# Performance work log

Hardware: AMD Instinct MI355X
Metric: run time of the kernel (lower is better)

Reference implementation:

```python
import jax, jax.numpy as jnp
import numpy as np


def setup_inputs() -> dict:
    key = jax.random.key(0)
    kx, kq, kk, kv = jax.random.split(key, 4)
    d_model, d_head = 1024, 64
    x = jax.random.normal(kx, (4, 4096, d_model), dtype=jnp.float32)
    scale = 1.0 / np.sqrt(d_model)
    Wq = jax.random.normal(kq, (d_model, d_head), dtype=jnp.float32) * scale
    Wk = jax.random.normal(kk, (d_model, d_head), dtype=jnp.float32) * scale
    Wv = jax.random.normal(kv, (d_model, d_head), dtype=jnp.float32) * scale
    return {"x": x, "Wq": Wq, "Wk": Wk, "Wv": Wv}


def reference(x, Wq, Wk, Wv):
    # x: [B, S, D]; Wq/Wk/Wv: [D, H]
    d_head = Wq.shape[-1]
    Q = jnp.einsum('bsd,dh->bsh', x, Wq)
    K = jnp.einsum('bsd,dh->bsh', x, Wk)
    V = jnp.einsum('bsd,dh->bsh', x, Wv)
    scores = jnp.einsum('bqh,bkh->bqk', Q, K) / jnp.sqrt(jnp.float32(d_head))
    S = x.shape[1]
    causal = jnp.tril(jnp.ones((S, S), dtype=bool))  # [S, S]
    scores = jnp.where(causal, scores, -jnp.inf)
    weights = jax.nn.softmax(scores, axis=-1)  # [B, S, S]
    return jnp.einsum('bqk,bkh->bqh', weights, V)
```

## Files before the change

### kernel.cpp

```cpp
#include <hip/hip_runtime.h>

#define D_MODEL 1024
#define D_HEAD  64
#define SEQ     4096
#define BATCH   4
#define M_TOT   (BATCH * SEQ)
#define LOG2E   1.44269504088896f
#define MFIX_L2 17.3123404906676f

typedef __bf16 bf16;
typedef bf16  bf16x8 __attribute__((ext_vector_type(8)));
typedef float f32x4  __attribute__((ext_vector_type(4)));

#define MFMA(a, b, c) __builtin_amdgcn_mfma_f32_16x16x32_bf16(a, b, c, 0, 0, 0)

#define QKV_OFF 0
#define OBUF_OFF 6291456
#define LBUF_OFF 10485760
#define WT_OFF   10551296

__global__ void zero_kernel(float4* __restrict__ p, int n4)
{
    int i = blockIdx.x * 256 + threadIdx.x;
    if (i < n4) p[i] = float4{0.f, 0.f, 0.f, 0.f};
}

__global__ void wt_kernel(const float* __restrict__ Wq, const float* __restrict__ Wk,
                          const float* __restrict__ Wv, bf16* __restrict__ Wt)
{
    const int bx = blockIdx.x;
    const int wm = bx >> 6, n = bx & 63;
    const float* W = (wm == 0) ? Wq : (wm == 1) ? Wk : Wv;
    #pragma unroll
    for (int j = 0; j < 4; j++) {
        int k = threadIdx.x + j * 256;
        Wt[(size_t)bx * D_MODEL + k] = (bf16)W[(size_t)k * D_HEAD + n];
    }
}

#define XP 40

__global__ __launch_bounds__(256) void proj_kernel(
    const float* __restrict__ x, const bf16* __restrict__ Wt,
    bf16* __restrict__ qkv)
{
    __shared__ __align__(16) bf16 xs[64][XP];
    __shared__ __align__(16) bf16 ws[192][XP];

    const int t    = threadIdx.x;
    const int wv   = t >> 6;
    const int lane = t & 63;
    const int quad = lane >> 4;
    const int l15  = lane & 15;
    const int bm   = blockIdx.x;

    const int xrow = t >> 2;
    const int xk8  = (t & 3) * 8;
    const float* xg = x + (size_t)(bm * 64 + xrow) * D_MODEL + xk8;

    f32x4 acc[12] = {};

    float4 xa = *(const float4*)(xg);
    float4 xb = *(const float4*)(xg + 4);

    for (int k0 = 0; k0 < D_MODEL; k0 += 32) {
        bf16x8 xv;
        xv[0] = (bf16)xa.x; xv[1] = (bf16)xa.y; xv[2] = (bf16)xa.z; xv[3] = (bf16)xa.w;
        xv[4] = (bf16)xb.x; xv[5] = (bf16)xb.y; xv[6] = (bf16)xb.z; xv[7] = (bf16)xb.w;
        *(bf16x8*)&xs[xrow][xk8] = xv;
        #pragma unroll
        for (int it = 0; it < 3; it++) {
            int id = t + it * 256;
            int n = id >> 2, kk8 = (id & 3) * 8;
            *(bf16x8*)&ws[n][kk8] =
                *(const bf16x8*)(Wt + (size_t)n * D_MODEL + k0 + kk8);
        }
        __syncthreads();

        if (k0 + 32 < D_MODEL) {
            xa = *(const float4*)(xg + k0 + 32);
            xb = *(const float4*)(xg + k0 + 36);
        }

        bf16x8 a = *(bf16x8*)&xs[wv * 16 + l15][quad * 8];
        #pragma unroll
        for (int t4 = 0; t4 < 12; t4++) {
            bf16x8 b = *(bf16x8*)&ws[t4 * 16 + l15][quad * 8];
            acc[t4] = MFMA(a, b, acc[t4]);
        }
        __syncthreads();
    }

    #pragma unroll
    for (int t4 = 0; t4 < 12; t4++) {
        const int wm = t4 >> 2;
        const float sc = (wm == 0) ? 0.125f : 1.0f;
        const int h = (t4 & 3) * 16 + l15;
        bf16* outp = qkv + (size_t)wm * M_TOT * D_HEAD;
        #pragma unroll
        for (int r = 0; r < 4; r++) {
            int m = bm * 64 + wv * 16 + quad * 4 + r;
            outp[(size_t)m * D_HEAD + h] = (bf16)(acc[t4][r] * sc);
        }
    }
}

#define TS 72

__global__ __launch_bounds__(256) void attn_kernel(
    const bf16* __restrict__ qkv, float* __restrict__ o_buf,
    float* __restrict__ l_buf)
{
    __shared__ __align__(16) bf16 Ks[64][TS];
    __shared__ __align__(16) bf16 Vs[64][TS];
    __shared__ __align__(16) bf16 Ps[4][16][TS];

    const int i = blockIdx.x;
    const int c = blockIdx.y;
    const int b = blockIdx.z;
    const int ntiles = i + 1;
    const int tile0  = c * 8;
    if (tile0 >= ntiles) return;
    const int tile1 = min(tile0 + 8, ntiles);

    const bf16* Q = qkv;
    const bf16* K = qkv + (size_t)M_TOT * D_HEAD;
    const bf16* V = qkv + (size_t)2 * M_TOT * D_HEAD;

    const int t    = threadIdx.x;
    const int wv   = t >> 6;
    const int lane = t & 63;
    const int quad = lane >> 4;
    const int l15  = lane & 15;
    const int qb   = i * 64;
    const size_t base = (size_t)b * SEQ * D_HEAD;

    bf16x8 qf0, qf1;
    {
        const bf16* qr = Q + base + (size_t)(qb + wv * 16 + l15) * D_HEAD;
        qf0 = *(const bf16x8*)(qr + quad * 8);
        qf1 = *(const bf16x8*)(qr + 32 + quad * 8);
    }

    f32x4 o[4] = {};
    float l_r[4] = {};
    const int qw0 = qb + wv * 16;

    const int krow = t >> 2;
    const int kq8  = (t & 3) * 8;
    const int vdim = t & 63;

    for (int tile = tile0; tile < tile1; tile++) {
        const int kk0 = tile * 64;
        {
            const bf16* kp = K + base + (size_t)(kk0 + krow) * D_HEAD;
            *(bf16x8*)&Ks[krow][kq8]      = *(const bf16x8*)(kp + kq8);
            *(bf16x8*)&Ks[krow][kq8 + 32] = *(const bf16x8*)(kp + kq8 + 32);
        }
        #pragma unroll
        for (int h = 0; h < 2; h++) {
            const int kk = (t >> 6) * 8 + h * 32;
            bf16x8 vvv;
            #pragma unroll
            for (int j = 0; j < 8; j++)
                vvv[j] = V[base + (size_t)(kk0 + kk + j) * D_HEAD + vdim];
            *(bf16x8*)&Vs[vdim][kk] = vvv;
        }
        __syncthreads();

        f32x4 sc4[4];
        #pragma unroll
        for (int kt = 0; kt < 4; kt++) {
            f32x4 z = {};
            z = MFMA(qf0, *(bf16x8*)&Ks[kt * 16 + l15][quad * 8],      z);
            z = MFMA(qf1, *(bf16x8*)&Ks[kt * 16 + l15][32 + quad * 8], z);
            sc4[kt] = z;
        }

        const bool need_mask = (tile == i);

        #pragma unroll
        for (int r = 0; r < 4; r++) {
            #pragma unroll
            for (int kt = 0; kt < 4; kt++) {
                float s = sc4[kt][r];
                if (need_mask && (kk0 + kt * 16 + l15 > qw0 + quad * 4 + r))
                    s = -1e30f;
                float p = __builtin_amdgcn_exp2f(fmaf(s, LOG2E, -MFIX_L2));
                l_r[r] += p;
                Ps[wv][quad * 4 + r][kt * 16 + l15] = (bf16)p;
            }
        }
        __syncthreads();

        #pragma unroll
        for (int c2 = 0; c2 < 2; c2++) {
            bf16x8 pa = *(bf16x8*)&Ps[wv][l15][c2 * 32 + quad * 8];
            #pragma unroll
            for (int t4 = 0; t4 < 4; t4++) {
                bf16x8 vb = *(bf16x8*)&Vs[t4 * 16 + l15][c2 * 32 + quad * 8];
                o[t4] = MFMA(pa, vb, o[t4]);
            }
        }
        __syncthreads();
    }

    const int mrow0 = b * SEQ + qw0;
    #pragma unroll
    for (int r = 0; r < 4; r++) {
        float ls = l_r[r];
        #pragma unroll
        for (int sh = 1; sh < 16; sh <<= 1)
            ls += __shfl_xor(ls, sh, 64);
        if (l15 == 0)
            atomicAdd(&l_buf[mrow0 + quad * 4 + r], ls);
        const size_t orow = (size_t)(mrow0 + quad * 4 + r) * D_HEAD;
        #pragma unroll
        for (int t4 = 0; t4 < 4; t4++)
            atomicAdd(&o_buf[orow + t4 * 16 + l15], o[t4][r]);
    }
}

__global__ void norm_kernel(const float4* __restrict__ o_buf,
                            const float* __restrict__ l_buf,
                            float4* __restrict__ out)
{
    int gid = blockIdx.x * 256 + threadIdx.x;
    int m = gid >> 4;
    float inv = 1.0f / l_buf[m];
    float4 v = o_buf[gid];
    out[gid] = float4{v.x * inv, v.y * inv, v.z * inv, v.w * inv};
}

extern "C" void kernel_launch(void* const* d_in, const int* in_sizes, int n_in,
                              void* d_out, int out_size, void* d_ws, size_t ws_size,
                              hipStream_t stream) {
    const float* x  = (const float*)d_in[0];
    const float* Wq = (const float*)d_in[1];
    const float* Wk = (const float*)d_in[2];
    const float* Wv = (const float*)d_in[3];

    bf16*  qkv   = (bf16*)((char*)d_ws + QKV_OFF);
    float* o_buf = (float*)((char*)d_ws + OBUF_OFF);
    float* l_buf = (float*)((char*)d_ws + LBUF_OFF);
    bf16*  Wt    = (bf16*)((char*)d_ws + WT_OFF);

    const int zero4 = (M_TOT * 65) / 4;
    zero_kernel<<<(zero4 + 255) / 256, 256, 0, stream>>>((float4*)o_buf, zero4);
    wt_kernel<<<192, 256, 0, stream>>>(Wq, Wk, Wv, Wt);
    proj_kernel<<<M_TOT / 64, 256, 0, stream>>>(x, Wt, qkv);
    attn_kernel<<<dim3(SEQ / 64, 8, BATCH), 256, 0, stream>>>(qkv, o_buf, l_buf);
    norm_kernel<<<M_TOT * 16 / 256, 256, 0, stream>>>((const float4*)o_buf, l_buf,
                                                      (float4*)d_out);
}
```

Baseline: 173.0 us.

## Drop LDS from projection and shrink attention KV chunk for more blocks

The projection kernel becomes a single-wavefront block over 16 rows. Weight fragments are loaded straight from global memory into registers with a one-step prefetch, which removes the shared-memory staging and barriers. The attention split-KV chunk drops from 8 to 4 tiles, and the grid's y dimension grows to 16 so more blocks run in parallel. The cost is that each projection block rereads the full weight matrix from cache, and the smaller chunks mean more atomic adds into the output and row-sum buffers.

```diff
diff --git a/kernel.cpp b/kernel.cpp
--- a/kernel.cpp
+++ b/kernel.cpp
@@ -7,6 +7,7 @@
 #define M_TOT   (BATCH * SEQ)
 #define LOG2E   1.44269504088896f
 #define MFIX_L2 17.3123404906676f
+#define CHUNK   4
 
 typedef __bf16 bf16;
 typedef bf16  bf16x8 __attribute__((ext_vector_type(8)));
@@ -38,57 +39,48 @@
     }
 }
 
-#define XP 40
-
-__global__ __launch_bounds__(256) void proj_kernel(
+__global__ __launch_bounds__(64) void proj_kernel(
     const float* __restrict__ x, const bf16* __restrict__ Wt,
     bf16* __restrict__ qkv)
 {
-    __shared__ __align__(16) bf16 xs[64][XP];
-    __shared__ __align__(16) bf16 ws[192][XP];
-
-    const int t    = threadIdx.x;
-    const int wv   = t >> 6;
-    const int lane = t & 63;
+    const int lane = threadIdx.x;
     const int quad = lane >> 4;
     const int l15  = lane & 15;
-    const int bm   = blockIdx.x;
-
-    const int xrow = t >> 2;
-    const int xk8  = (t & 3) * 8;
-    const float* xg = x + (size_t)(bm * 64 + xrow) * D_MODEL + xk8;
+    const int row0 = blockIdx.x * 16;
+
+    const float* xr = x + (size_t)(row0 + l15) * D_MODEL + quad * 8;
+    const bf16*  wp = Wt + (size_t)l15 * D_MODEL + quad * 8;
 
     f32x4 acc[12] = {};
 
-    float4 xa = *(const float4*)(xg);
-    float4 xb = *(const float4*)(xg + 4);
+    float4 xa = *(const float4*)(xr);
+    float4 xb = *(const float4*)(xr + 4);
+    bf16x8 bf[12];
+    #pragma unroll
+    for (int t4 = 0; t4 < 12; t4++)
+        bf[t4] = *(const bf16x8*)(wp + (size_t)(t4 * 16) * D_MODEL);
 
     for (int k0 = 0; k0 < D_MODEL; k0 += 32) {
-        bf16x8 xv;
-        xv[0] = (bf16)xa.x; xv[1] = (bf16)xa.y; xv[2] = (bf16)xa.z; xv[3] = (bf16)xa.w;
-        xv[4] = (bf16)xb.x; xv[5] = (bf16)xb.y; xv[6] = (bf16)xb.z; xv[7] = (bf16)xb.w;
-        *(bf16x8*)&xs[xrow][xk8] = xv;
-        #pragma unroll
-        for (int it = 0; it < 3; it++) {
-            int id = t + it * 256;
-            int n = id >> 2, kk8 = (id & 3) * 8;
-            *(bf16x8*)&ws[n][kk8] =
-                *(const bf16x8*)(Wt + (size_t)n * D_MODEL + k0 + kk8);
-        }
-        __syncthreads();
-
-        if (k0 + 32 < D_MODEL) {
-            xa = *(const float4*)(xg + k0 + 32);
-            xb = *(const float4*)(xg + k0 + 36);
-        }
-
-        bf16x8 a = *(bf16x8*)&xs[wv * 16 + l15][quad * 8];
-        #pragma unroll
-        for (int t4 = 0; t4 < 12; t4++) {
-            bf16x8 b = *(bf16x8*)&ws[t4 * 16 + l15][quad * 8];
-            acc[t4] = MFMA(a, b, acc[t4]);
-        }
-        __syncthreads();
+        bf16x8 a;
+        a[0] = (bf16)xa.x; a[1] = (bf16)xa.y; a[2] = (bf16)xa.z; a[3] = (bf16)xa.w;
+        a[4] = (bf16)xb.x; a[5] = (bf16)xb.y; a[6] = (bf16)xb.z; a[7] = (bf16)xb.w;
+
+        bf16x8 bn[12];
+        const int k1 = k0 + 32;
+        if (k1 < D_MODEL) {
+            xa = *(const float4*)(xr + k1);
+            xb = *(const float4*)(xr + k1 + 4);
+            #pragma unroll
+            for (int t4 = 0; t4 < 12; t4++)
+                bn[t4] = *(const bf16x8*)(wp + (size_t)(t4 * 16) * D_MODEL + k1);
+        }
+
+        #pragma unroll
+        for (int t4 = 0; t4 < 12; t4++)
+            acc[t4] = MFMA(a, bf[t4], acc[t4]);
+
+        #pragma unroll
+        for (int t4 = 0; t4 < 12; t4++) bf[t4] = bn[t4];
     }
 
     #pragma unroll
@@ -99,7 +91,7 @@
         bf16* outp = qkv + (size_t)wm * M_TOT * D_HEAD;
         #pragma unroll
         for (int r = 0; r < 4; r++) {
-            int m = bm * 64 + wv * 16 + quad * 4 + r;
+            int m = row0 + quad * 4 + r;
             outp[(size_t)m * D_HEAD + h] = (bf16)(acc[t4][r] * sc);
         }
     }
@@ -111,17 +103,17 @@
     const bf16* __restrict__ qkv, float* __restrict__ o_buf,
     float* __restrict__ l_buf)
 {
-    __shared__ __align__(16) bf16 Ks[64][TS];
-    __shared__ __align__(16) bf16 Vs[64][TS];
-    __shared__ __align__(16) bf16 Ps[4][16][TS];
-
     const int i = blockIdx.x;
     const int c = blockIdx.y;
     const int b = blockIdx.z;
     const int ntiles = i + 1;
-    const int tile0  = c * 8;
+    const int tile0  = c * CHUNK;
     if (tile0 >= ntiles) return;
-    const int tile1 = min(tile0 + 8, ntiles);
+    const int tile1 = min(tile0 + CHUNK, ntiles);
+
+    __shared__ __align__(16) bf16 Ks[64][TS];
+    __shared__ __align__(16) bf16 Vs[64][TS];
+    __shared__ __align__(16) bf16 Ps[4][16][TS];
 
     const bf16* Q = qkv;
     const bf16* K = qkv + (size_t)M_TOT * D_HEAD;
@@ -248,8 +240,9 @@
     const int zero4 = (M_TOT * 65) / 4;
     zero_kernel<<<(zero4 + 255) / 256, 256, 0, stream>>>((float4*)o_buf, zero4);
     wt_kernel<<<192, 256, 0, stream>>>(Wq, Wk, Wv, Wt);
-    proj_kernel<<<M_TOT / 64, 256, 0, stream>>>(x, Wt, qkv);
-    attn_kernel<<<dim3(SEQ / 64, 8, BATCH), 256, 0, stream>>>(qkv, o_buf, l_buf);
+    proj_kernel<<<M_TOT / 16, 64, 0, stream>>>(x, Wt, qkv);
+    attn_kernel<<<dim3(SEQ / 64, SEQ / 64 / CHUNK, BATCH), 256, 0, stream>>>(
+        qkv, o_buf, l_buf);
     norm_kernel<<<M_TOT * 16 / 256, 256, 0, stream>>>((const float4*)o_buf, l_buf,
                                                       (float4*)d_out);
 }
```

New measurement: 195.9 us. 1.13x slower.
